# Optimization experiments

Hardware: AMD Instinct MI355X
Metric: run time of the kernel (lower is better)

## Reference

```python
import jax, jax.numpy as jnp
import numpy as np

B, S, D_IN, D_OUT, RANK = 4, 2048, 4096, 4096, 16
SCALING = 32.0 / RANK  # alpha / rank
MASK_DENSITY = 0.01


def setup_inputs() -> dict:
    key = jax.random.key(0)
    ks = jax.random.split(key, 7)
    x = jax.random.normal(ks[0], (B, S, D_IN), dtype=jnp.float32)
    W = jax.random.normal(ks[1], (D_OUT, D_IN), dtype=jnp.float32) / np.sqrt(D_IN)
    b = jax.random.normal(ks[2], (D_OUT,), dtype=jnp.float32) * 0.01
    lora_A = jax.random.normal(ks[3], (RANK, D_IN), dtype=jnp.float32) / np.sqrt(D_IN)
    lora_B = jax.random.normal(ks[4], (D_OUT, RANK), dtype=jnp.float32) * 0.01
    delta = jax.random.normal(ks[5], (D_OUT, D_IN), dtype=jnp.float32) * 0.01
    mask = jax.random.bernoulli(ks[6], MASK_DENSITY, (D_OUT, D_IN))
    return {"x": x, "W": W, "b": b, "lora_A": lora_A, "lora_B": lora_B,
            "delta": delta, "mask": mask}


def reference(x, W, b, lora_A, lora_B, delta, mask):
    # frozen linear: [B,S,D_in] @ [D_in,D_out] + b
    out = jnp.einsum("bsd,od->bso", x, W) + b
    # LoRA branch: (x @ A^T) @ B^T * scaling
    out = out + jnp.einsum("bsr,or->bso", jnp.einsum("bsd,rd->bsr", x, lora_A), lora_B) * SCALING
    # sparse delta branch: F.linear(x, delta * mask)
    masked_delta = delta * mask.astype(delta.dtype)
    out = out + jnp.einsum("bsd,od->bso", x, masked_delta)
    return out
```

## Files before the change

kernel.cpp:

```cpp
#include <hip/hip_runtime.h>
#include <hip/hip_bf16.h>

typedef __hip_bfloat16 bf16;
typedef __attribute__((ext_vector_type(8))) short bf16x8;
typedef __attribute__((ext_vector_type(4))) float f32x4;
typedef __attribute__((ext_vector_type(4))) int int4v;

#define AS1 __attribute__((address_space(1)))
#define AS3 __attribute__((address_space(3)))

#define MDIM 8192
#define NDIM 4096
#define KDIM 4096
#define SCALING 2.0f
#define NT (KDIM / 64)

__global__ __launch_bounds__(256) void prep(
    const float* __restrict__ W, const float* __restrict__ lA,
    const float* __restrict__ lB, const float* __restrict__ delta,
    const int* __restrict__ mask, bf16* __restrict__ Weff,
    const float* __restrict__ X, bf16* __restrict__ Xb)
{
    const int bid = blockIdx.x;
    if (bid < 8192) {
        int idx = bid * 256 + threadIdx.x;
        int o   = idx >> 9;
        int d0  = (idx & 511) << 3;
        size_t base = (size_t)o * KDIM + d0;

        float Bo[16];
#pragma unroll
        for (int r = 0; r < 16; ++r) Bo[r] = lB[o * 16 + r];

        f32x4 wa = *(const f32x4*)(W + base);
        f32x4 wb = *(const f32x4*)(W + base + 4);
        f32x4 da = *(const f32x4*)(delta + base);
        f32x4 db = *(const f32x4*)(delta + base + 4);

        int mk[8];
        *(int4v*)(mk)     = *(const int4v*)(mask + base);
        *(int4v*)(mk + 4) = *(const int4v*)(mask + base + 4);

        float lor[8] = {0.f, 0.f, 0.f, 0.f, 0.f, 0.f, 0.f, 0.f};
#pragma unroll
        for (int r = 0; r < 16; ++r) {
            f32x4 aa = *(const f32x4*)(lA + (size_t)r * KDIM + d0);
            f32x4 ab = *(const f32x4*)(lA + (size_t)r * KDIM + d0 + 4);
#pragma unroll
            for (int e = 0; e < 4; ++e) {
                lor[e]     += Bo[r] * aa[e];
                lor[e + 4] += Bo[r] * ab[e];
            }
        }

        int4v ov4;
        bf16* ov = (bf16*)&ov4;
#pragma unroll
        for (int e = 0; e < 8; ++e) {
            float w = (e < 4) ? wa[e] : wb[e - 4];
            float d = (e < 4) ? da[e] : db[e - 4];
            float a = w + SCALING * lor[e];
            if (mk[e]) a += d;
            ov[e] = __float2bfloat16(a);
        }
        *(int4v*)(Weff + base) = ov4;
    } else {
        size_t i = ((size_t)(bid - 8192) * 256 + threadIdx.x) * 8;
        f32x4 a = *(const f32x4*)(X + i);
        f32x4 b = *(const f32x4*)(X + i + 4);
        int4v ov4;
        bf16* ov = (bf16*)&ov4;
#pragma unroll
        for (int e = 0; e < 4; ++e) {
            ov[e]     = __float2bfloat16(a[e]);
            ov[e + 4] = __float2bfloat16(b[e]);
        }
        *(int4v*)(Xb + i) = ov4;
    }
}

__device__ __forceinline__ void stage_half(
    const bf16* __restrict__ g, int grow0, bf16* l, int half, int kt,
    int tid, int wvb)
{
    const int k0 = (kt < NT) ? kt * 64 : 0;
#pragma unroll
    for (int gi = 0; gi < 2; ++gi) {
        const int c  = gi * 512 + tid;
        const int ml = c >> 3;
        const int kc = (c & 7) ^ (ml & 7);
        __builtin_amdgcn_global_load_lds(
            (const AS1 void*)(g + (size_t)(grow0 + half * 128 + ml) * KDIM + k0 + kc * 8),
            (AS3 void*)(l + half * 8192 + (gi * 512 + wvb) * 8),
            16, 0, 0);
    }
}

#define RD_A(i) { const int m_ = wm * 128 + (i) * 16 + l16;                       \
    a[i][0] = *(const bf16x8*)(Ac + m_ * 64 + ((quad       ^ (m_ & 7)) * 8));     \
    a[i][1] = *(const bf16x8*)(Ac + m_ * 64 + (((4 + quad) ^ (m_ & 7)) * 8)); }
#define RD_B(j) { const int n_ = wn * 64 + (j) * 16 + l16;                        \
    b[j][0] = *(const bf16x8*)(Bc + n_ * 64 + ((quad       ^ (n_ & 7)) * 8));     \
    b[j][1] = *(const bf16x8*)(Bc + n_ * 64 + (((4 + quad) ^ (n_ & 7)) * 8)); }
#define MF2(i, j)                                                                 \
    acc[i][j] = __builtin_amdgcn_mfma_f32_16x16x32_bf16(a[i][0], b[j][0], acc[i][j], 0, 0, 0); \
    acc[i][j] = __builtin_amdgcn_mfma_f32_16x16x32_bf16(a[i][1], b[j][1], acc[i][j], 0, 0, 0);

__global__ __launch_bounds__(512, 2) void gemm_bf16_256(
    const bf16* __restrict__ X, const bf16* __restrict__ Wt,
    const float* __restrict__ bias, float* __restrict__ out)
{
    __shared__ bf16 As[2][256 * 64];
    __shared__ bf16 Bs[2][256 * 64];

    const int tid  = threadIdx.x;
    const int lane = tid & 63;
    const int wvb  = tid & ~63;
    const int wave = tid >> 6;
    const int wm   = wave & 1;
    const int wn   = wave >> 1;
    const int quad = lane >> 4;
    const int l16  = lane & 15;

    int idb = blockIdx.y * gridDim.x + blockIdx.x;
    idb = (idb & 7) * 64 + (idb >> 3);
    const int bn = (idb & 15) * 256;
    const int bm = (idb >> 4) * 256;

    f32x4 acc[8][4];
#pragma unroll
    for (int i = 0; i < 8; ++i)
#pragma unroll
        for (int j = 0; j < 4; ++j)
            acc[i][j] = (f32x4){0.f, 0.f, 0.f, 0.f};

    stage_half(X,  bm, As[0], 0, 0, tid, wvb);
    stage_half(X,  bm, As[0], 1, 0, tid, wvb);
    stage_half(Wt, bn, Bs[0], 0, 0, tid, wvb);
    stage_half(Wt, bn, Bs[0], 1, 0, tid, wvb);
    stage_half(X,  bm, As[1], 0, 1, tid, wvb);
    stage_half(X,  bm, As[1], 1, 1, tid, wvb);
    asm volatile("s_waitcnt vmcnt(4)" ::: "memory");
    __builtin_amdgcn_s_barrier();

    bf16x8 a[8][2], b[4][2];

    for (int t = 0; t < NT; ++t) {
        const int cur = t & 1;
        const bf16* Ac = As[cur];
        const bf16* Bc = Bs[cur];

        RD_A(0) RD_A(1) RD_A(2) RD_A(3)
        RD_B(0) RD_B(1)
        stage_half(Wt, bn, Bs[cur ^ 1], 0, t + 1, tid, wvb);
        __builtin_amdgcn_s_barrier();
        __builtin_amdgcn_s_setprio(1);
        MF2(0,0) MF2(1,0) MF2(2,0) MF2(3,0)
        MF2(0,1) MF2(1,1) MF2(2,1) MF2(3,1)
        __builtin_amdgcn_s_setprio(0);
        __builtin_amdgcn_s_barrier();

        RD_A(4) RD_A(5) RD_A(6) RD_A(7)
        stage_half(Wt, bn, Bs[cur ^ 1], 1, t + 1, tid, wvb);
        __builtin_amdgcn_s_barrier();
        __builtin_amdgcn_s_setprio(1);
        MF2(4,0) MF2(5,0) MF2(6,0) MF2(7,0)
        MF2(4,1) MF2(5,1) MF2(6,1) MF2(7,1)
        __builtin_amdgcn_s_setprio(0);
        __builtin_amdgcn_s_barrier();

        RD_B(2) RD_B(3)
        stage_half(X, bm, As[cur], 0, t + 2, tid, wvb);
        __builtin_amdgcn_s_barrier();
        __builtin_amdgcn_s_setprio(1);
        MF2(0,2) MF2(1,2) MF2(2,2) MF2(3,2)
        MF2(0,3) MF2(1,3) MF2(2,3) MF2(3,3)
        __builtin_amdgcn_s_setprio(0);
        __builtin_amdgcn_s_barrier();

        stage_half(X, bm, As[cur], 1, t + 2, tid, wvb);
        __builtin_amdgcn_s_barrier();
        __builtin_amdgcn_s_setprio(1);
        MF2(4,2) MF2(5,2) MF2(6,2) MF2(7,2)
        MF2(4,3) MF2(5,3) MF2(6,3) MF2(7,3)
        __builtin_amdgcn_s_setprio(0);
        asm volatile("s_waitcnt vmcnt(4)" ::: "memory");
        __builtin_amdgcn_s_barrier();
    }

    float bv[4];
#pragma unroll
    for (int j = 0; j < 4; ++j)
        bv[j] = bias[bn + wn * 64 + j * 16 + l16];

#pragma unroll
    for (int i = 0; i < 8; ++i) {
        const int mg = bm + wm * 128 + i * 16 + quad * 4;
#pragma unroll
        for (int j = 0; j < 4; ++j) {
            const int ng = bn + wn * 64 + j * 16 + l16;
#pragma unroll
            for (int r = 0; r < 4; ++r)
                out[(size_t)(mg + r) * NDIM + ng] = acc[i][j][r] + bv[j];
        }
    }
}

__global__ __launch_bounds__(256, 3) void gemm_f32(
    const float* __restrict__ X, const bf16* __restrict__ Wt,
    const float* __restrict__ bias, float* __restrict__ out)
{
    __shared__ float Asf[128 * 64];
    __shared__ bf16  Bs[128 * 64];

    const int tid  = threadIdx.x;
    const int lane = tid & 63;
    const int wave = tid >> 6;
    const int wmf  = wave & 1;
    const int wnf  = wave >> 1;
    const int quad = lane >> 4;
    const int l16  = lane & 15;

    const int bn = blockIdx.x * 128;
    const int bm = blockIdx.y * 128;
    const int cwave = tid & ~63;

    f32x4 acc[4][4];
#pragma unroll
    for (int i = 0; i < 4; ++i)
#pragma unroll
        for (int j = 0; j < 4; ++j)
            acc[i][j] = (f32x4){0.f, 0.f, 0.f, 0.f};

    for (int kt = 0; kt < KDIM / 64; ++kt) {
        const int k0 = kt * 64;
        if (kt) __syncthreads();
#pragma unroll
        for (int j = 0; j < 8; ++j) {
            const int c  = j * 256 + tid;
            const int m  = c >> 4;
            const int kc = (c & 15) ^ (m & 15);
            const int cb = j * 256 + cwave;
            __builtin_amdgcn_global_load_lds(
                (const AS1 void*)(X + (size_t)(bm + m) * KDIM + k0 + kc * 4),
                (AS3 void*)(Asf + cb * 4), 16, 0, 0);
        }
#pragma unroll
        for (int j = 0; j < 4; ++j) {
            const int c  = j * 256 + tid;
            const int m  = c >> 3;
            const int kc = (c & 7) ^ (m & 7);
            const int cb = j * 256 + cwave;
            __builtin_amdgcn_global_load_lds(
                (const AS1 void*)(Wt + (size_t)(bn + m) * KDIM + k0 + kc * 8),
                (AS3 void*)(Bs + cb * 8), 16, 0, 0);
        }
        __syncthreads();

#pragma unroll
        for (int ks = 0; ks < 2; ++ks) {
            bf16x8 af[4], bfr[4];
#pragma unroll
            for (int i = 0; i < 4; ++i) {
                const int m  = wmf * 64 + i * 16 + l16;
                const int k2 = (ks * 4 + quad) * 2;
                f32x4 lo = *(const f32x4*)(Asf + m * 64 + ((k2     ^ (m & 15)) * 4));
                f32x4 hi = *(const f32x4*)(Asf + m * 64 + (((k2+1) ^ (m & 15)) * 4));
                bf16 tmp[8];
#pragma unroll
                for (int e = 0; e < 4; ++e) {
                    tmp[e]     = __float2bfloat16(lo[e]);
                    tmp[e + 4] = __float2bfloat16(hi[e]);
                }
                af[i] = *(const bf16x8*)tmp;

                const int n   = wnf * 64 + i * 16 + l16;
                const int kcb = (ks * 4 + quad) ^ (n & 7);
                bfr[i] = *(const bf16x8*)(Bs + n * 64 + kcb * 8);
            }
#pragma unroll
            for (int i = 0; i < 4; ++i)
#pragma unroll
                for (int j = 0; j < 4; ++j)
                    acc[i][j] = __builtin_amdgcn_mfma_f32_16x16x32_bf16(
                        af[i], bfr[j], acc[i][j], 0, 0, 0);
        }
    }

    float bv[4];
#pragma unroll
    for (int j = 0; j < 4; ++j)
        bv[j] = bias[bn + wnf * 64 + j * 16 + l16];

#pragma unroll
    for (int i = 0; i < 4; ++i) {
        const int mg = bm + wmf * 64 + i * 16 + quad * 4;
#pragma unroll
        for (int j = 0; j < 4; ++j) {
            const int ng = bn + wnf * 64 + j * 16 + l16;
#pragma unroll
            for (int r = 0; r < 4; ++r)
                out[(size_t)(mg + r) * NDIM + ng] = acc[i][j][r] + bv[j];
        }
    }
}

extern "C" void kernel_launch(void* const* d_in, const int* in_sizes, int n_in,
                              void* d_out, int out_size, void* d_ws, size_t ws_size,
                              hipStream_t stream)
{
    const float* x     = (const float*)d_in[0];
    const float* W     = (const float*)d_in[1];
    const float* b     = (const float*)d_in[2];
    const float* lA    = (const float*)d_in[3];
    const float* lB    = (const float*)d_in[4];
    const float* delta = (const float*)d_in[5];
    const int*   mask  = (const int*)d_in[6];
    float* out = (float*)d_out;

    bf16* Weff = (bf16*)d_ws;
    bf16* Xb   = (bf16*)((char*)d_ws + (size_t)NDIM * KDIM * 2);

    const size_t need = (size_t)NDIM * KDIM * 2 + (size_t)MDIM * KDIM * 2;

    if (ws_size >= need) {
        prep<<<dim3(8192 + 16384), 256, 0, stream>>>(
            W, lA, lB, delta, mask, Weff, x, Xb);
        gemm_bf16_256<<<dim3(NDIM / 256, MDIM / 256), 512, 0, stream>>>(
            Xb, Weff, b, out);
    } else {
        prep<<<dim3(8192), 256, 0, stream>>>(
            W, lA, lB, delta, mask, Weff, x, Xb);
        gemm_f32<<<dim3(NDIM / 128, MDIM / 128), 256, 0, stream>>>(
            x, Weff, b, out);
    }
}
```

Before: 678.0 us.

## Split MFMA phases by K-half and prefetch next tile's fragments across iterations

```diff
diff --git a/kernel.cpp b/kernel.cpp
--- a/kernel.cpp
+++ b/kernel.cpp
@@ -96,15 +96,12 @@
     }
 }
 
-#define RD_A(i) { const int m_ = wm * 128 + (i) * 16 + l16;                       \
-    a[i][0] = *(const bf16x8*)(Ac + m_ * 64 + ((quad       ^ (m_ & 7)) * 8));     \
-    a[i][1] = *(const bf16x8*)(Ac + m_ * 64 + (((4 + quad) ^ (m_ & 7)) * 8)); }
-#define RD_B(j) { const int n_ = wn * 64 + (j) * 16 + l16;                        \
-    b[j][0] = *(const bf16x8*)(Bc + n_ * 64 + ((quad       ^ (n_ & 7)) * 8));     \
-    b[j][1] = *(const bf16x8*)(Bc + n_ * 64 + (((4 + quad) ^ (n_ & 7)) * 8)); }
-#define MF2(i, j)                                                                 \
-    acc[i][j] = __builtin_amdgcn_mfma_f32_16x16x32_bf16(a[i][0], b[j][0], acc[i][j], 0, 0, 0); \
-    acc[i][j] = __builtin_amdgcn_mfma_f32_16x16x32_bf16(a[i][1], b[j][1], acc[i][j], 0, 0, 0);
+#define FENCE asm volatile("" ::: "memory")
+
+#define RD_A(arr, i, ks, P) { const int m_ = wm * 128 + (i) * 16 + l16;           \
+    arr[i] = *(const bf16x8*)((P) + m_ * 64 + ((((ks) * 4 + quad) ^ (m_ & 7)) * 8)); }
+#define RD_B(arr, j, ks, P) { const int n_ = wn * 64 + (j) * 16 + l16;            \
+    arr[j] = *(const bf16x8*)((P) + n_ * 64 + ((((ks) * 4 + quad) ^ (n_ & 7)) * 8)); }
 
 __global__ __launch_bounds__(512, 2) void gemm_bf16_256(
     const bf16* __restrict__ X, const bf16* __restrict__ Wt,
@@ -142,49 +139,89 @@
     stage_half(X,  bm, As[1], 1, 1, tid, wvb);
     asm volatile("s_waitcnt vmcnt(4)" ::: "memory");
     __builtin_amdgcn_s_barrier();
-
-    bf16x8 a[8][2], b[4][2];
+    FENCE;
+
+    bf16x8 aK0[8], aK1[8], bK0[4], bK1[4];
+
+#pragma unroll
+    for (int i = 0; i < 4; ++i) RD_A(aK0, i, 0, As[0]);
+#pragma unroll
+    for (int j = 0; j < 4; ++j) RD_B(bK0, j, 0, Bs[0]);
 
     for (int t = 0; t < NT; ++t) {
         const int cur = t & 1;
         const bf16* Ac = As[cur];
         const bf16* Bc = Bs[cur];
-
-        RD_A(0) RD_A(1) RD_A(2) RD_A(3)
-        RD_B(0) RD_B(1)
+        const bf16* An = As[cur ^ 1];
+        const bf16* Bn = Bs[cur ^ 1];
+
+#pragma unroll
+        for (int i = 4; i < 8; ++i) RD_A(aK0, i, 0, Ac);
+#pragma unroll
+        for (int i = 0; i < 4; ++i) RD_A(aK1, i, 1, Ac);
         stage_half(Wt, bn, Bs[cur ^ 1], 0, t + 1, tid, wvb);
+        FENCE;
         __builtin_amdgcn_s_barrier();
         __builtin_amdgcn_s_setprio(1);
-        MF2(0,0) MF2(1,0) MF2(2,0) MF2(3,0)
-        MF2(0,1) MF2(1,1) MF2(2,1) MF2(3,1)
+#pragma unroll
+        for (int i = 0; i < 4; ++i)
+#pragma unroll
+            for (int j = 0; j < 4; ++j)
+                acc[i][j] = __builtin_amdgcn_mfma_f32_16x16x32_bf16(
+                    aK0[i], bK0[j], acc[i][j], 0, 0, 0);
         __builtin_amdgcn_s_setprio(0);
-        __builtin_amdgcn_s_barrier();
-
-        RD_A(4) RD_A(5) RD_A(6) RD_A(7)
+        FENCE;
+        __builtin_amdgcn_s_barrier();
+
+#pragma unroll
+        for (int j = 0; j < 4; ++j) RD_B(bK1, j, 1, Bc);
+#pragma unroll
+        for (int i = 4; i < 8; ++i) RD_A(aK1, i, 1, Ac);
         stage_half(Wt, bn, Bs[cur ^ 1], 1, t + 1, tid, wvb);
+        FENCE;
         __builtin_amdgcn_s_barrier();
         __builtin_amdgcn_s_setprio(1);
-        MF2(4,0) MF2(5,0) MF2(6,0) MF2(7,0)
-        MF2(4,1) MF2(5,1) MF2(6,1) MF2(7,1)
+#pragma unroll
+        for (int i = 4; i < 8; ++i)
+#pragma unroll
+            for (int j = 0; j < 4; ++j)
+                acc[i][j] = __builtin_amdgcn_mfma_f32_16x16x32_bf16(
+                    aK0[i], bK0[j], acc[i][j], 0, 0, 0);
         __builtin_amdgcn_s_setprio(0);
-        __builtin_amdgcn_s_barrier();
-
-        RD_B(2) RD_B(3)
+        FENCE;
+        __builtin_amdgcn_s_barrier();
+
         stage_half(X, bm, As[cur], 0, t + 2, tid, wvb);
+        stage_half(X, bm, As[cur], 1, t + 2, tid, wvb);
+        FENCE;
         __builtin_amdgcn_s_barrier();
         __builtin_amdgcn_s_setprio(1);
-        MF2(0,2) MF2(1,2) MF2(2,2) MF2(3,2)
-        MF2(0,3) MF2(1,3) MF2(2,3) MF2(3,3)
+#pragma unroll
+        for (int i = 0; i < 4; ++i)
+#pragma unroll
+            for (int j = 0; j < 4; ++j)
+                acc[i][j] = __builtin_amdgcn_mfma_f32_16x16x32_bf16(
+                    aK1[i], bK1[j], acc[i][j], 0, 0, 0);
         __builtin_amdgcn_s_setprio(0);
-        __builtin_amdgcn_s_barrier();
-
-        stage_half(X, bm, As[cur], 1, t + 2, tid, wvb);
-        __builtin_amdgcn_s_barrier();
+        FENCE;
+        __builtin_amdgcn_s_barrier();
+
+        asm volatile("s_waitcnt vmcnt(4)" ::: "memory");
+        __builtin_amdgcn_s_barrier();
+        FENCE;
+#pragma unroll
+        for (int i = 0; i < 4; ++i) RD_A(aK0, i, 0, An);
+#pragma unroll
+        for (int j = 0; j < 4; ++j) RD_B(bK0, j, 0, Bn);
         __builtin_amdgcn_s_setprio(1);
-        MF2(4,2) MF2(5,2) MF2(6,2) MF2(7,2)
-        MF2(4,3) MF2(5,3) MF2(6,3) MF2(7,3)
+#pragma unroll
+        for (int i = 4; i < 8; ++i)
+#pragma unroll
+            for (int j = 0; j < 4; ++j)
+                acc[i][j] = __builtin_amdgcn_mfma_f32_16x16x32_bf16(
+                    aK1[i], bK1[j], acc[i][j], 0, 0, 0);
         __builtin_amdgcn_s_setprio(0);
-        asm volatile("s_waitcnt vmcnt(4)" ::: "memory");
+        FENCE;
         __builtin_amdgcn_s_barrier();
     }
 
```

Measured after the change: 667.1 us. Within noise of the previous version (-1.6%).
